# Optimization experiments

Measured on AMD Instinct MI355X. Metric: run time of the kernel, lower is better.

## Reference

```python
import jax, jax.numpy as jnp
import numpy as np

WIN = 32  # hardcoded window size in the original module


def _find(parent, x):
    while parent[x] != x:
        parent[x] = parent[parent[x]]
        x = parent[x]
    return x


def _label_background(bg):
    # 4-connected component labeling of True pixels; False pixels get label 0
    w = bg.shape[0]
    n = w * w
    parent = np.arange(n, dtype=np.int64)
    flat = bg.ravel()
    idx = np.arange(n).reshape(w, w)
    e1 = np.concatenate([idx[:, :-1].ravel(), idx[:-1, :].ravel()])
    e2 = np.concatenate([idx[:, 1:].ravel(), idx[1:, :].ravel()])
    for a, b in zip(e1, e2):
        if flat[a] and flat[b]:
            ra, rb = _find(parent, a), _find(parent, b)
            if ra != rb:
                parent[ra] = rb
    labels = np.zeros(n, dtype=np.int64)
    root2lab = {}
    nxt = 1
    for i in range(n):
        if flat[i]:
            r = _find(parent, i)
            if r not in root2lab:
                root2lab[r] = nxt
                nxt += 1
            labels[i] = root2lab[r]
    return labels


def _malis(seg, e1, e2, costs, pos):
    # Kruskal-style maximin MALIS edge weighting (descending affinity order).
    # Pairs involving segment label 0 (foreground / non-background) are excluded.
    n = seg.shape[0]
    parent = np.arange(n, dtype=np.int64)
    cnts = [({int(seg[i]): 1} if seg[i] != 0 else {}) for i in range(n)]
    w = np.zeros(costs.shape[0], dtype=np.int64)
    order = np.argsort(-costs, kind='stable')
    for e in order:
        a, b = _find(parent, e1[e]), _find(parent, e2[e])
        if a == b:
            continue
        ca, cb = cnts[a], cnts[b]
        if len(ca) > len(cb):  # small-to-large merge
            a, b, ca, cb = b, a, cb, ca
        common = 0
        for l, c in ca.items():
            if l in cb:
                common += c * cb[l]
        if pos:
            w[e] = common
        else:
            sa = sum(ca.values())
            sb = sum(cb.values())
            w[e] = sa * sb - common
        for l, c in ca.items():
            cb[l] = cb.get(l, 0) + c
        parent[a] = b
        cnts[a] = {}
    return w


def _malis_weights_full(pred, target):
    pred = np.asarray(pred)
    target = np.asarray(target)
    B, C, H, W = pred.shape
    weights_n = np.zeros(pred.shape, dtype=np.float32)
    weights_p = np.zeros(pred.shape, dtype=np.float32)
    idx = np.arange(WIN * WIN).reshape(WIN, WIN)
    e1 = np.concatenate([idx[:, :-1].ravel(), idx[:-1, :].ravel()])
    e2 = np.concatenate([idx[:, 1:].ravel(), idx[1:, :].ravel()])
    for r in range(H // WIN):
        for c in range(W // WIN):
            p = pred[:, :, r * WIN:(r + 1) * WIN, c * WIN:(c + 1) * WIN]
            t = target[:, :, r * WIN:(r + 1) * WIN, c * WIN:(c + 1) * WIN]
            costs_h = (p[:, :, :, :-1] + p[:, :, :, 1:]).reshape(B, -1)
            costs_v = (p[:, :, :-1, :] + p[:, :, 1:, :]).reshape(B, -1)
            costs = np.concatenate([costs_h, costs_v], 1)
            gt_h = (t[:, :, :, :-1] + t[:, :, :, 1:]).reshape(B, -1)
            gt_v = (t[:, :, :-1, :] + t[:, :, 1:, :]).reshape(B, -1)
            gt = np.concatenate([gt_h, gt_v], 1)
            costs_n = costs.copy()
            costs_p = costs.copy()
            costs_n[gt > 20] = 20
            costs_p[gt < 10] = 0
            gt = np.minimum(gt, 20)
            for i in range(B):
                seg = _label_background(t[i, 0] == 0)
                wn = _malis(seg, e1, e2, costs_n[i].astype(np.float32), 0).astype(np.float64)
                wp = _malis(seg, e1, e2, costs_p[i].astype(np.float32), 1).astype(np.float64)
                if wn.sum() > 0:
                    wn = wn / wn.sum()
                if wp.sum() > 0:
                    wp = wp / wp.sum()
                wn[gt[i] >= 10] = 0
                wp[gt[i] < 20] = 0
                half = WIN * (WIN - 1)
                for wsrc, wdst in ((wn, weights_n), (wp, weights_p)):
                    wh = wsrc[:half].reshape(WIN, WIN - 1)
                    wv = wsrc[half:].reshape(WIN - 1, WIN)
                    nw = np.zeros((WIN, WIN), dtype=np.float64)
                    nw[:, :-1] += wh
                    nw[:, 1:] += wh
                    nw[:-1, :] += wv
                    nw[1:, :] += wv
                    wdst[i, 0, r * WIN:(r + 1) * WIN, c * WIN:(c + 1) * WIN] = nw
    return weights_n, weights_p


def setup_inputs() -> dict:
    key = jax.random.key(0)
    k1, k2 = jax.random.split(key)
    y_true = jax.random.randint(k1, (4, 1, 256, 256), 0, 2).astype(jnp.float32) * 20.0
    y_pred = jax.random.uniform(k2, (4, 1, 256, 256), dtype=jnp.float32) * 20.0
    return {"y_true": y_true, "y_pred": y_pred}


def reference(y_true, y_pred):
    malis_lr = 1.0
    malis_lr_pos = 1.0
    out_sd = (jax.ShapeDtypeStruct(y_pred.shape, jnp.float32),
              jax.ShapeDtypeStruct(y_pred.shape, jnp.float32))
    weights_n, weights_p = jax.pure_callback(
        _malis_weights_full, out_sd,
        jax.lax.stop_gradient(y_pred), jax.lax.stop_gradient(y_true))
    loss_n = y_pred ** 2
    loss_p = (20.0 - y_pred) ** 2
    return (malis_lr * loss_n * weights_n + malis_lr_pos * loss_p * weights_p).sum()
```

## Files before the change

### kernel.cpp

```cpp
#include <hip/hip_runtime.h>

#define NPIX   1024
#define NEH    992
#define NEDGE  1984
#define SORTN  2048
#define CHUNK  8
#define NMERGE 1023
#define NIL    0xFFFFu

#define MRG_STRIDE 20480
#define MRG_M      0
#define MRG_RA     256
#define MRG_RB     4608
#define MRG_SS     8960
#define MRG_ED     13312
#define MRG_NXT    15616

__device__ __forceinline__ void edge_ab(int e, int& a, int& b) {
    if (e < NEH) { int y = e / 31; int x = e - y * 31; a = y * 32 + x; b = a + 1; }
    else         { int ev = e - NEH; a = ev; b = ev + 32; }
}

__device__ __forceinline__ uint4 add4(uint4 x, uint4 y) {
    return make_uint4(x.x + y.x, x.y + y.y, x.z + y.z, x.w + y.w);
}
__device__ __forceinline__ uint4 sub4(uint4 x, uint4 y) {
    return make_uint4(x.x - y.x, x.y - y.y, x.z - y.z, x.w - y.w);
}

__device__ void ccl_body(char* smem, int* kprimeSh,
                         const float* __restrict__ t_glob,
                         unsigned short* __restrict__ pixLab_g,
                         int* __restrict__ Kg, int tileId) {
    const int tid = threadIdx.x;
    const int bat = tileId >> 6;
    const int tile = tileId & 63;
    const int tr = tile >> 3, tc = tile & 7;

    unsigned short* labS = (unsigned short*)smem;
    unsigned int*   cntS = (unsigned int*)(smem + 2048);
    unsigned char*  bgS  = (unsigned char*)(smem + 20480);

    for (int i = tid; i < NPIX; i += 256) {
        int y = i >> 5, x = i & 31;
        int gidx = bat * 65536 + (tr * 32 + y) * 256 + (tc * 32 + x);
        bgS[i] = (t_glob[gidx] == 0.0f) ? 1 : 0;
    }
    __syncthreads();

    if (tid < 64) {
        const int lane = tid;
        if (lane < 32) {
            #pragma unroll
            for (int x = 0; x < 32; x++) {
                int i = lane * 32 + x;
                labS[i] = bgS[i] ? (unsigned short)i : (unsigned short)NIL;
            }
        }
        while (true) {
            bool changed = false;
            if (lane < 32) {
                const int base = lane * 32;
                unsigned short v[32];
                #pragma unroll
                for (int x = 0; x < 32; x++) v[x] = labS[base + x];
                unsigned run = NIL;
                #pragma unroll
                for (int x = 0; x < 32; x++) {
                    unsigned val = v[x];
                    if (val == NIL) { run = NIL; }
                    else { unsigned nv = min(run, val); changed |= (nv != val); v[x] = (unsigned short)nv; run = nv; }
                }
                run = NIL;
                #pragma unroll
                for (int x = 31; x >= 0; x--) {
                    unsigned val = v[x];
                    if (val == NIL) { run = NIL; }
                    else { unsigned nv = min(run, val); changed |= (nv != val); v[x] = (unsigned short)nv; run = nv; }
                }
                #pragma unroll
                for (int x = 0; x < 32; x++) labS[base + x] = v[x];
            }
            if (lane < 32) {
                unsigned short c[32];
                #pragma unroll
                for (int k = 0; k < 32; k++) c[k] = labS[k * 32 + lane];
                unsigned run = NIL;
                #pragma unroll
                for (int k = 0; k < 32; k++) {
                    unsigned val = c[k];
                    if (val == NIL) { run = NIL; }
                    else { unsigned nv = min(run, val); changed |= (nv != val); c[k] = (unsigned short)nv; run = nv; }
                }
                run = NIL;
                #pragma unroll
                for (int k = 31; k >= 0; k--) {
                    unsigned val = c[k];
                    if (val == NIL) { run = NIL; }
                    else { unsigned nv = min(run, val); changed |= (nv != val); c[k] = (unsigned short)nv; run = nv; }
                }
                #pragma unroll
                for (int k = 0; k < 32; k++) labS[k * 32 + lane] = c[k];
            }
            if (!__any(changed)) break;
        }
    }
    __syncthreads();

    for (int i = tid; i < NPIX; i += 256) cntS[i] = 0;
    if (tid == 0) *kprimeSh = 0;
    __syncthreads();
    for (int i = tid; i < NPIX; i += 256)
        if (bgS[i]) atomicAdd(&cntS[labS[i]], 1u);
    __syncthreads();
    for (int i = tid; i < NPIX; i += 256) {
        if (bgS[i] && (int)labS[i] == i) {
            unsigned id = (cntS[i] >= 2) ? (unsigned)atomicAdd(kprimeSh, 1) : NIL;
            cntS[i] = id;
        }
    }
    __syncthreads();
    for (int i = tid; i < NPIX; i += 256)
        pixLab_g[tileId * NPIX + i] = bgS[i] ? (unsigned short)cntS[labS[i]] : (unsigned short)NIL;
    if (tid == 0) Kg[tileId] = *kprimeSh;
}

__device__ void sort_body(char* smem,
                          const float* __restrict__ t_glob,
                          const float* __restrict__ p_glob,
                          unsigned short* __restrict__ ord_g, int wg) {
    const int tid = threadIdx.x;
    const int sgn = wg & 1;
    const int tileId = wg >> 1;
    const int bat = tileId >> 6;
    const int tile = tileId & 63;
    const int tr = tile >> 3, tc = tile & 7;

    float*              pT   = (float*)smem;
    unsigned long long* keys = (unsigned long long*)(smem + 4096);
    unsigned char*      bgS  = (unsigned char*)(smem + 20480);

    for (int i = tid; i < NPIX; i += 256) {
        int y = i >> 5, x = i & 31;
        int gidx = bat * 65536 + (tr * 32 + y) * 256 + (tc * 32 + x);
        pT[i] = p_glob[gidx];
        bgS[i] = (t_glob[gidx] == 0.0f) ? 1 : 0;
    }
    __syncthreads();

    for (int k = tid; k < SORTN; k += 256) {
        unsigned long long key = 0ULL;
        if (k < NEDGE) {
            int a, b; edge_ab(k, a, b);
            float cost = pT[a] + pT[b];
            int nfg = (int)(!bgS[a]) + (int)(!bgS[b]);
            if (sgn == 0) { if (nfg == 2) cost = 20.0f; }
            else          { if (nfg == 0) cost = 0.0f;  }
            key = ((unsigned long long)__float_as_uint(cost) << 16)
                | (unsigned long long)(0xFFFFu - (unsigned)k);
        }
        keys[k] = key;
    }
    __syncthreads();
    for (int kk = 2; kk <= SORTN; kk <<= 1) {
        for (int jj = kk >> 1; jj > 0; jj >>= 1) {
            for (int i = tid; i < SORTN; i += 256) {
                int ixj = i ^ jj;
                if (ixj > i) {
                    unsigned long long A = keys[i], Bv = keys[ixj];
                    bool descBlk = ((i & kk) == 0);
                    if ((A < Bv) == descBlk) { keys[i] = Bv; keys[ixj] = A; }
                }
            }
            __syncthreads();
        }
    }
    for (int k = tid; k < NEDGE; k += 256)
        ord_g[(size_t)wg * SORTN + k] = (unsigned short)(0xFFFFu - (unsigned)(keys[k] & 0xFFFFULL));
}

__global__ __launch_bounds__(256, 2)
void k12_ccl_sort(const float* __restrict__ t_glob,
                  const float* __restrict__ p_glob,
                  unsigned short* __restrict__ pixLab_g,
                  int* __restrict__ Kg,
                  unsigned short* __restrict__ ord_g,
                  int nT) {
    __shared__ __align__(16) char smem[21504];
    __shared__ int kprimeSh;
    if ((int)blockIdx.x < nT)
        ccl_body(smem, &kprimeSh, t_glob, pixLab_g, Kg, blockIdx.x);
    else
        sort_body(smem, t_glob, p_glob, ord_g, blockIdx.x - nT);
}

__global__ __launch_bounds__(64)
void k3_kruskal(const float* __restrict__ t_glob,
                const unsigned short* __restrict__ ord_g,
                char* __restrict__ mrg_base) {
    const int lane = threadIdx.x;
    const int wg  = blockIdx.x;
    const int tileId = wg >> 1;
    const int bat = tileId >> 6;
    const int tile = tileId & 63;
    const int tr = tile >> 3, tc = tile & 7;

    __shared__ unsigned short parentS[NPIX];
    __shared__ unsigned long long nodeS[NPIX];
    __shared__ unsigned short nextS[NPIX];
    __shared__ unsigned int   claimS[NPIX];

    char* mg = mrg_base + (size_t)wg * MRG_STRIDE;
    unsigned int*   mrA = (unsigned int*)(mg + MRG_RA);
    unsigned int*   mrB = (unsigned int*)(mg + MRG_RB);
    unsigned int*   mSS = (unsigned int*)(mg + MRG_SS);
    unsigned short* mED = (unsigned short*)(mg + MRG_ED);
    unsigned short* mNX = (unsigned short*)(mg + MRG_NXT);
    const unsigned short* ord = ord_g + (size_t)wg * SORTN;

    for (int i = lane; i < NPIX; i += 64) {
        int y = i >> 5, x = i & 31;
        int gidx = bat * 65536 + (tr * 32 + y) * 256 + (tc * 32 + x);
        unsigned bg = (t_glob[gidx] == 0.0f) ? 1u : 0u;
        parentS[i] = (unsigned short)i;
        nodeS[i] = ((unsigned long long)i << 48) | ((unsigned long long)i << 32)
                 | (1ULL << 16) | (unsigned long long)bg;
        nextS[i] = (unsigned short)NIL;
    }
    __syncthreads();

    int m = 0;
    for (int kb = 0; kb < NEDGE; kb += 64) {
        int e = ord[kb + lane];
        int a, b; edge_ab(e, a, b);
        unsigned ra = (unsigned)a, rb = (unsigned)b;
        bool pending = true;
        bool committed = false;
        unsigned recA = 0, recB = 0, recSS = 0;

        while (__any(pending)) {
            if (pending) {
                while (true) {
                    unsigned pa = parentS[ra];
                    unsigned pb = parentS[rb];
                    if (pa == ra && pb == rb) break;
                    if (pa != ra) { unsigned ga = parentS[pa]; parentS[ra] = (unsigned short)ga; ra = ga; }
                    if (pb != rb) { unsigned gb = parentS[pb]; parentS[rb] = (unsigned short)gb; rb = gb; }
                }
                if (ra == rb) pending = false;
            }
            if (pending) {
                claimS[ra] = 0xFFFFFFFFu;
                claimS[rb] = 0xFFFFFFFFu;
            }
            if (pending) {
                atomicMin(&claimS[ra], (unsigned)lane);
                atomicMin(&claimS[rb], (unsigned)lane);
            }
            bool win = pending && (claimS[ra] == (unsigned)lane) && (claimS[rb] == (unsigned)lane);
            if (win) {
                unsigned long long nA = nodeS[ra], nB = nodeS[rb];
                unsigned cons = ra, surv = rb;
                unsigned szAu = (unsigned)(nA >> 16) & 0xFFFFu;
                unsigned szBu = (unsigned)(nB >> 16) & 0xFFFFu;
                if (szAu > szBu) {
                    unsigned t = cons; cons = surv; surv = t;
                    unsigned long long tn = nA; nA = nB; nB = tn;
                }
                unsigned headA = (unsigned)(nA >> 48);
                unsigned tailA = (unsigned)(nA >> 32) & 0xFFFFu;
                unsigned szA   = (unsigned)(nA >> 16) & 0xFFFFu;
                unsigned slA   = (unsigned)nA & 0xFFFFu;
                unsigned headB = (unsigned)(nB >> 48);
                unsigned tailB = (unsigned)(nB >> 32) & 0xFFFFu;
                unsigned szB   = (unsigned)(nB >> 16) & 0xFFFFu;
                unsigned slB   = (unsigned)nB & 0xFFFFu;
                unsigned long long merged =
                      ((unsigned long long)headA << 48)
                    | ((unsigned long long)tailB << 32)
                    | ((unsigned long long)(szA + szB) << 16)
                    | (unsigned long long)(slA + slB);
                parentS[cons] = (unsigned short)surv;
                nodeS[surv]   = merged;
                nextS[tailA]  = (unsigned short)headB;
                recA = (headA << 16) | headB;
                recB = (szA << 16) | szB;
                recSS = slA * slB;
                committed = true;
                pending = false;
            }
        }
        unsigned long long cm = __ballot(committed);
        if (committed) {
            int idx = m + (int)__popcll(cm & ((1ULL << lane) - 1ULL));
            mrA[idx] = recA;
            mrB[idx] = recB;
            mSS[idx] = recSS;
            mED[idx] = (unsigned short)e;
        }
        m += (int)__popcll(cm);
    }
    if (lane == 0) *(int*)(mg + MRG_M) = m;
    for (int i = lane; i < NPIX; i += 64) mNX[i] = nextS[i];
}

__global__ __launch_bounds__(256, 2)
void k4_weights(const float* __restrict__ t_glob,
                const float* __restrict__ p_glob,
                const unsigned short* __restrict__ pixLab_g,
                const int* __restrict__ Kg,
                const char* __restrict__ mrg_base,
                float* __restrict__ out) {
    const int tid = threadIdx.x;
    const int wg  = blockIdx.x;
    const int sgn = wg & 1;
    const int tileId = wg >> 1;
    const int bat = tileId >> 6;
    const int tile = tileId & 63;
    const int tr = tile >> 3, tc = tile & 7;

    __shared__ float          pT[NPIX];
    __shared__ unsigned char  bgS[NPIX];
    __shared__ unsigned short pixLab[NPIX];
    __shared__ unsigned short posS[NPIX];
    __shared__ unsigned int   mRecA[NMERGE];
    __shared__ unsigned int   mRecB[NMERGE];
    __shared__ unsigned int   mSaSb[NMERGE];
    __shared__ unsigned int   commonW[NMERGE];
    __shared__ unsigned short mEd[NMERGE];
    __shared__ __align__(16) unsigned long long big[2564];
    __shared__ unsigned wsumSh;
    __shared__ float lossSh;

    const char* mg = mrg_base + (size_t)wg * MRG_STRIDE;
    const int M = *(const int*)(mg + MRG_M);
    const int K = Kg[tileId];
    const unsigned int*   mrA = (const unsigned int*)(mg + MRG_RA);
    const unsigned int*   mrB = (const unsigned int*)(mg + MRG_RB);
    const unsigned int*   mSS = (const unsigned int*)(mg + MRG_SS);
    const unsigned short* mED = (const unsigned short*)(mg + MRG_ED);
    const unsigned short* mNX = (const unsigned short*)(mg + MRG_NXT);

    for (int i = tid; i < NPIX; i += 256) {
        int y = i >> 5, x = i & 31;
        int gidx = bat * 65536 + (tr * 32 + y) * 256 + (tc * 32 + x);
        pT[i] = p_glob[gidx];
        bgS[i] = (t_glob[gidx] == 0.0f) ? 1 : 0;
        pixLab[i] = pixLab_g[tileId * NPIX + i];
    }
    for (int j = tid; j < M; j += 256) {
        mRecA[j] = mrA[j];
        mRecB[j] = mrB[j];
        mSaSb[j] = mSS[j];
        mEd[j]   = mED[j];
        commonW[j] = 0;
    }

    unsigned short* n0 = (unsigned short*)big;
    unsigned short* n1 = n0 + 1024;
    unsigned short* d0 = n0 + 2048;
    unsigned short* d1 = n0 + 3072;
    for (int i = tid; i < NPIX; i += 256) { n0[i] = mNX[i]; d0[i] = 1; }
    __syncthreads();
    for (int s = 0; s < 10; s++) {
        unsigned short* sn = (s & 1) ? n1 : n0;
        unsigned short* sd = (s & 1) ? d1 : d0;
        unsigned short* dn = (s & 1) ? n0 : n1;
        unsigned short* dd = (s & 1) ? d0 : d1;
        for (int i = tid; i < NPIX; i += 256) {
            unsigned nx = sn[i];
            unsigned dv = sd[i];
            if (nx != NIL) { dv += sd[nx]; nx = sn[nx]; }
            dn[i] = (unsigned short)nx;
            dd[i] = (unsigned short)dv;
        }
        __syncthreads();
    }
    for (int i = tid; i < NPIX; i += 256)
        posS[i] = (unsigned short)(NPIX - (int)d0[i]);
    __syncthreads();

    unsigned*       P32 = (unsigned*)big;
    uint4*          P4  = (uint4*)big;
    unsigned*       scr = P32 + 4100;
    uint4*          S4  = (uint4*)scr;
    unsigned short* P16 = (unsigned short*)big;
    for (int base = 0; base < K; base += CHUNK) {
        for (int idx = tid; idx < 4100; idx += 256) P32[idx] = 0;
        __syncthreads();
        for (int i = tid; i < NPIX; i += 256) {
            unsigned l = pixLab[i];
            if (l != NIL && l >= (unsigned)base && l < (unsigned)(base + CHUNK))
                P16[(posS[i] + 1) * 8 + (l - base)] = 1;
        }
        __syncthreads();
        {
            int r0 = tid * 4 + 1;
            uint4 acc = P4[r0];
            for (int rr = r0 + 1; rr <= r0 + 3; rr++) { acc = add4(acc, P4[rr]); P4[rr] = acc; }
            S4[tid] = acc;
            __syncthreads();
            if (tid < 64) {
                uint4 s0 = S4[tid * 4], s1 = S4[tid * 4 + 1], s2 = S4[tid * 4 + 2], s3 = S4[tid * 4 + 3];
                uint4 t1 = add4(s0, s1), t2 = add4(t1, s2), t3 = add4(t2, s3);
                uint4 run = t3;
                #pragma unroll
                for (int d = 1; d < 64; d <<= 1) {
                    uint4 o;
                    o.x = __shfl_up(run.x, d, 64);
                    o.y = __shfl_up(run.y, d, 64);
                    o.z = __shfl_up(run.z, d, 64);
                    o.w = __shfl_up(run.w, d, 64);
                    if (tid >= d) run = add4(run, o);
                }
                uint4 off = sub4(run, t3);
                S4[tid * 4]     = add4(s0, off);
                S4[tid * 4 + 1] = add4(t1, off);
                S4[tid * 4 + 2] = add4(t2, off);
                S4[tid * 4 + 3] = add4(t3, off);
            }
            __syncthreads();
            if (tid > 0) {
                uint4 off = S4[tid - 1];
                for (int rr = r0; rr <= r0 + 3; rr++) P4[rr] = add4(P4[rr], off);
            }
        }
        __syncthreads();
        for (int j = tid; j < M; j += 256) {
            unsigned recA = mRecA[j], recB = mRecB[j];
            unsigned aS = posS[recA >> 16];
            unsigned bS = posS[recA & 0xFFFFu];
            uint4 da = sub4(P4[aS + (recB >> 16)], P4[aS]);
            uint4 db = sub4(P4[bS + (recB & 0xFFFFu)], P4[bS]);
            unsigned acc;
            acc  = (da.x & 0xFFFFu) * (db.x & 0xFFFFu) + (da.x >> 16) * (db.x >> 16);
            acc += (da.y & 0xFFFFu) * (db.y & 0xFFFFu) + (da.y >> 16) * (db.y >> 16);
            acc += (da.z & 0xFFFFu) * (db.z & 0xFFFFu) + (da.z >> 16) * (db.z >> 16);
            acc += (da.w & 0xFFFFu) * (db.w & 0xFFFFu) + (da.w >> 16) * (db.w >> 16);
            commonW[j] += acc;
        }
        __syncthreads();
    }

    if (tid == 0) { wsumSh = 0; lossSh = 0.0f; }
    __syncthreads();
    unsigned wloc = 0;
    for (int j = tid; j < M; j += 256)
        wloc += (sgn == 0) ? (mSaSb[j] - commonW[j]) : commonW[j];
    if (wloc) atomicAdd(&wsumSh, wloc);
    __syncthreads();
    const unsigned wsum = wsumSh;
    if (wsum > 0) {
        const double inv = 1.0 / (double)wsum;
        float lloc = 0.0f;
        for (int j = tid; j < M; j += 256) {
            unsigned w = (sgn == 0) ? (mSaSb[j] - commonW[j]) : commonW[j];
            if (!w) continue;
            int e = mEd[j];
            int a, b; edge_ab(e, a, b);
            int nfg = (int)(!bgS[a]) + (int)(!bgS[b]);
            bool keep = (sgn == 0) ? (nfg == 0) : (nfg >= 1);
            if (!keep) continue;
            float wn = (float)((double)w * inv);
            float fa, fb;
            if (sgn == 0) { fa = pT[a] * pT[a];            fb = pT[b] * pT[b]; }
            else { float da = 20.0f - pT[a], db = 20.0f - pT[b]; fa = da * da; fb = db * db; }
            lloc += wn * (fa + fb);
        }
        if (lloc != 0.0f) atomicAdd(&lossSh, lloc);
        __syncthreads();
        if (tid == 0 && lossSh != 0.0f) atomicAdd(out, lossSh);
    }
}

__global__ __launch_bounds__(256, 2)
void malis_mono(const float* __restrict__ t_glob,
                const float* __restrict__ p_glob,
                float* __restrict__ out) {
    const int tid  = threadIdx.x;
    const int wg   = blockIdx.x;
    const int sgn  = wg & 1;
    const int tileId = wg >> 1;
    const int bat  = tileId >> 6;
    const int tile = tileId & 63;
    const int tr = tile >> 3, tc = tile & 7;

    __shared__ float          pT[NPIX];
    __shared__ unsigned char  bgS[NPIX];
    __shared__ unsigned short pixLab[NPIX];
    __shared__ unsigned short parentS[NPIX];
    __shared__ unsigned short nextS[NPIX];
    __shared__ unsigned long long nodeS[NPIX];
    __shared__ unsigned int   claimS[NPIX];
    __shared__ unsigned short posS[NPIX];
    __shared__ unsigned short orderS[NEDGE];
    __shared__ unsigned int   mRecA[NMERGE];
    __shared__ unsigned int   mRecB[NMERGE];
    __shared__ unsigned short mEd[NMERGE];
    __shared__ unsigned int   mSaSb[NMERGE];
    __shared__ unsigned int   commonW[NMERGE];
    __shared__ __align__(16) unsigned long long big[2564];
    __shared__ int   kprimeSh, mCountSh;
    __shared__ unsigned wsumSh;
    __shared__ float lossSh;

    for (int i = tid; i < NPIX; i += 256) {
        int y = i >> 5, x = i & 31;
        int gidx = bat * 65536 + (tr * 32 + y) * 256 + (tc * 32 + x);
        pT[i] = p_glob[gidx];
        bgS[i] = (t_glob[gidx] == 0.0f) ? 1 : 0;
    }
    __syncthreads();

    unsigned short* labS = (unsigned short*)big;
    unsigned int*   cntS = (unsigned int*)(((char*)big) + 2048);
    if (tid < 64) {
        const int lane = tid;
        if (lane < 32) {
            #pragma unroll
            for (int x = 0; x < 32; x++) {
                int i = lane * 32 + x;
                labS[i] = bgS[i] ? (unsigned short)i : (unsigned short)NIL;
            }
        }
        while (true) {
            bool changed = false;
            if (lane < 32) {
                const int base = lane * 32;
                unsigned short v[32];
                #pragma unroll
                for (int x = 0; x < 32; x++) v[x] = labS[base + x];
                unsigned run = NIL;
                #pragma unroll
                for (int x = 0; x < 32; x++) {
                    unsigned val = v[x];
                    if (val == NIL) { run = NIL; }
                    else { unsigned nv = min(run, val); changed |= (nv != val); v[x] = (unsigned short)nv; run = nv; }
                }
                run = NIL;
                #pragma unroll
                for (int x = 31; x >= 0; x--) {
                    unsigned val = v[x];
                    if (val == NIL) { run = NIL; }
                    else { unsigned nv = min(run, val); changed |= (nv != val); v[x] = (unsigned short)nv; run = nv; }
                }
                #pragma unroll
                for (int x = 0; x < 32; x++) labS[base + x] = v[x];
            }
            if (lane < 32) {
                unsigned short c[32];
                #pragma unroll
                for (int k = 0; k < 32; k++) c[k] = labS[k * 32 + lane];
                unsigned run = NIL;
                #pragma unroll
                for (int k = 0; k < 32; k++) {
                    unsigned val = c[k];
                    if (val == NIL) { run = NIL; }
                    else { unsigned nv = min(run, val); changed |= (nv != val); c[k] = (unsigned short)nv; run = nv; }
                }
                run = NIL;
                #pragma unroll
                for (int k = 31; k >= 0; k--) {
                    unsigned val = c[k];
                    if (val == NIL) { run = NIL; }
                    else { unsigned nv = min(run, val); changed |= (nv != val); c[k] = (unsigned short)nv; run = nv; }
                }
                #pragma unroll
                for (int k = 0; k < 32; k++) labS[k * 32 + lane] = c[k];
            }
            if (!__any(changed)) break;
        }
    }
    __syncthreads();

    for (int i = tid; i < NPIX; i += 256) cntS[i] = 0;
    if (tid == 0) kprimeSh = 0;
    __syncthreads();
    for (int i = tid; i < NPIX; i += 256)
        if (bgS[i]) atomicAdd(&cntS[labS[i]], 1u);
    __syncthreads();
    for (int i = tid; i < NPIX; i += 256) {
        if (bgS[i] && (int)labS[i] == i) {
            unsigned id = (cntS[i] >= 2) ? (unsigned)atomicAdd(&kprimeSh, 1) : NIL;
            cntS[i] = id;
        }
    }
    __syncthreads();
    for (int i = tid; i < NPIX; i += 256)
        pixLab[i] = bgS[i] ? (unsigned short)cntS[labS[i]] : (unsigned short)NIL;
    __syncthreads();
    const int K = kprimeSh;

    unsigned long long* keys = big;
    for (int k = tid; k < SORTN; k += 256) {
        unsigned long long key = 0ULL;
        if (k < NEDGE) {
            int a, b; edge_ab(k, a, b);
            float cost = pT[a] + pT[b];
            int nfg = (int)(!bgS[a]) + (int)(!bgS[b]);
            if (sgn == 0) { if (nfg == 2) cost = 20.0f; }
            else          { if (nfg == 0) cost = 0.0f;  }
            key = ((unsigned long long)__float_as_uint(cost) << 16)
                | (unsigned long long)(0xFFFFu - (unsigned)k);
        }
        keys[k] = key;
    }
    __syncthreads();
    for (int kk = 2; kk <= SORTN; kk <<= 1) {
        for (int jj = kk >> 1; jj > 0; jj >>= 1) {
            for (int i = tid; i < SORTN; i += 256) {
                int ixj = i ^ jj;
                if (ixj > i) {
                    unsigned long long A = keys[i], Bv = keys[ixj];
                    bool descBlk = ((i & kk) == 0);
                    if ((A < Bv) == descBlk) { keys[i] = Bv; keys[ixj] = A; }
                }
            }
            __syncthreads();
        }
    }
    for (int k = tid; k < NEDGE; k += 256)
        orderS[k] = (unsigned short)(0xFFFFu - (unsigned)(keys[k] & 0xFFFFULL));
    for (int i = tid; i < NPIX; i += 256) {
        parentS[i] = (unsigned short)i;
        nodeS[i] = ((unsigned long long)i << 48) | ((unsigned long long)i << 32)
                 | (1ULL << 16) | (unsigned long long)bgS[i];
        nextS[i] = (unsigned short)NIL;
    }
    __syncthreads();

    if (tid < 64) {
        const int lane = tid;
        int m = 0;
        for (int kb = 0; kb < NEDGE; kb += 64) {
            int e = orderS[kb + lane];
            int a, b; edge_ab(e, a, b);
            unsigned ra = (unsigned)a, rb = (unsigned)b;
            bool pending = true;
            bool committed = false;
            unsigned recA = 0, recB = 0, recSS = 0;
            while (__any(pending)) {
                if (pending) {
                    while (true) {
                        unsigned pa = parentS[ra];
                        unsigned pb = parentS[rb];
                        if (pa == ra && pb == rb) break;
                        if (pa != ra) { unsigned ga = parentS[pa]; parentS[ra] = (unsigned short)ga; ra = ga; }
                        if (pb != rb) { unsigned gb = parentS[pb]; parentS[rb] = (unsigned short)gb; rb = gb; }
                    }
                    if (ra == rb) pending = false;
                }
                if (pending) {
                    claimS[ra] = 0xFFFFFFFFu;
                    claimS[rb] = 0xFFFFFFFFu;
                }
                if (pending) {
                    atomicMin(&claimS[ra], (unsigned)lane);
                    atomicMin(&claimS[rb], (unsigned)lane);
                }
                bool win = pending && (claimS[ra] == (unsigned)lane) && (claimS[rb] == (unsigned)lane);
                if (win) {
                    unsigned long long nA = nodeS[ra], nB = nodeS[rb];
                    unsigned cons = ra, surv = rb;
                    unsigned szAu = (unsigned)(nA >> 16) & 0xFFFFu;
                    unsigned szBu = (unsigned)(nB >> 16) & 0xFFFFu;
                    if (szAu > szBu) {
                        unsigned t = cons; cons = surv; surv = t;
                        unsigned long long tn = nA; nA = nB; nB = tn;
                    }
                    unsigned headA = (unsigned)(nA >> 48);
                    unsigned tailA = (unsigned)(nA >> 32) & 0xFFFFu;
                    unsigned szA   = (unsigned)(nA >> 16) & 0xFFFFu;
                    unsigned slA   = (unsigned)nA & 0xFFFFu;
                    unsigned headB = (unsigned)(nB >> 48);
                    unsigned tailB = (unsigned)(nB >> 32) & 0xFFFFu;
                    unsigned szB   = (unsigned)(nB >> 16) & 0xFFFFu;
                    unsigned slB   = (unsigned)nB & 0xFFFFu;
                    unsigned long long merged =
                          ((unsigned long long)headA << 48)
                        | ((unsigned long long)tailB << 32)
                        | ((unsigned long long)(szA + szB) << 16)
                        | (unsigned long long)(slA + slB);
                    parentS[cons] = (unsigned short)surv;
                    nodeS[surv]   = merged;
                    nextS[tailA]  = (unsigned short)headB;
                    recA = (headA << 16) | headB;
                    recB = (szA << 16) | szB;
                    recSS = slA * slB;
                    committed = true;
                    pending = false;
                }
            }
            unsigned long long cm = __ballot(committed);
            if (committed) {
                int idx = m + (int)__popcll(cm & ((1ULL << lane) - 1ULL));
                mRecA[idx] = recA;
                mRecB[idx] = recB;
                mSaSb[idx] = recSS;
                mEd[idx]   = (unsigned short)e;
            }
            m += (int)__popcll(cm);
        }
        if (lane == 0) mCountSh = m;
    }
    __syncthreads();
    const int M = mCountSh;
    for (int j = tid; j < M; j += 256) commonW[j] = 0;

    unsigned short* n0 = (unsigned short*)big;
    unsigned short* n1 = n0 + 1024;
    unsigned short* d0 = n0 + 2048;
    unsigned short* d1 = n0 + 3072;
    for (int i = tid; i < NPIX; i += 256) { n0[i] = nextS[i]; d0[i] = 1; }
    __syncthreads();
    for (int s = 0; s < 10; s++) {
        unsigned short* sn = (s & 1) ? n1 : n0;
        unsigned short* sd = (s & 1) ? d1 : d0;
        unsigned short* dn = (s & 1) ? n0 : n1;
        unsigned short* dd = (s & 1) ? d0 : d1;
        for (int i = tid; i < NPIX; i += 256) {
            unsigned nx = sn[i];
            unsigned dv = sd[i];
            if (nx != NIL) { dv += sd[nx]; nx = sn[nx]; }
            dn[i] = (unsigned short)nx;
            dd[i] = (unsigned short)dv;
        }
        __syncthreads();
    }
    for (int i = tid; i < NPIX; i += 256)
        posS[i] = (unsigned short)(NPIX - (int)d0[i]);
    __syncthreads();

    unsigned*       P32 = (unsigned*)big;
    uint4*          P4  = (uint4*)big;
    unsigned*       scr = P32 + 4100;
    uint4*          S4  = (uint4*)scr;
    unsigned short* P16 = (unsigned short*)big;
    for (int base = 0; base < K; base += CHUNK) {
        for (int idx = tid; idx < 4100; idx += 256) P32[idx] = 0;
        __syncthreads();
        for (int i = tid; i < NPIX; i += 256) {
            unsigned l = pixLab[i];
            if (l != NIL && l >= (unsigned)base && l < (unsigned)(base + CHUNK))
                P16[(posS[i] + 1) * 8 + (l - base)] = 1;
        }
        __syncthreads();
        {
            int r0 = tid * 4 + 1;
            uint4 acc = P4[r0];
            for (int rr = r0 + 1; rr <= r0 + 3; rr++) { acc = add4(acc, P4[rr]); P4[rr] = acc; }
            S4[tid] = acc;
            __syncthreads();
            if (tid < 64) {
                uint4 s0 = S4[tid * 4], s1 = S4[tid * 4 + 1], s2 = S4[tid * 4 + 2], s3 = S4[tid * 4 + 3];
                uint4 t1 = add4(s0, s1), t2 = add4(t1, s2), t3 = add4(t2, s3);
                uint4 run = t3;
                #pragma unroll
                for (int d = 1; d < 64; d <<= 1) {
                    uint4 o;
                    o.x = __shfl_up(run.x, d, 64);
                    o.y = __shfl_up(run.y, d, 64);
                    o.z = __shfl_up(run.z, d, 64);
                    o.w = __shfl_up(run.w, d, 64);
                    if (tid >= d) run = add4(run, o);
                }
                uint4 off = sub4(run, t3);
                S4[tid * 4]     = add4(s0, off);
                S4[tid * 4 + 1] = add4(t1, off);
                S4[tid * 4 + 2] = add4(t2, off);
                S4[tid * 4 + 3] = add4(t3, off);
            }
            __syncthreads();
            if (tid > 0) {
                uint4 off = S4[tid - 1];
                for (int rr = r0; rr <= r0 + 3; rr++) P4[rr] = add4(P4[rr], off);
            }
        }
        __syncthreads();
        for (int j = tid; j < M; j += 256) {
            unsigned recA = mRecA[j], recB = mRecB[j];
            unsigned aS = posS[recA >> 16];
            unsigned bS = posS[recA & 0xFFFFu];
            uint4 da = sub4(P4[aS + (recB >> 16)], P4[aS]);
            uint4 db = sub4(P4[bS + (recB & 0xFFFFu)], P4[bS]);
            unsigned acc;
            acc  = (da.x & 0xFFFFu) * (db.x & 0xFFFFu) + (da.x >> 16) * (db.x >> 16);
            acc += (da.y & 0xFFFFu) * (db.y & 0xFFFFu) + (da.y >> 16) * (db.y >> 16);
            acc += (da.z & 0xFFFFu) * (db.z & 0xFFFFu) + (da.z >> 16) * (db.z >> 16);
            acc += (da.w & 0xFFFFu) * (db.w & 0xFFFFu) + (da.w >> 16) * (db.w >> 16);
            commonW[j] += acc;
        }
        __syncthreads();
    }

    if (tid == 0) { wsumSh = 0; lossSh = 0.0f; }
    __syncthreads();
    unsigned wloc = 0;
    for (int j = tid; j < M; j += 256)
        wloc += (sgn == 0) ? (mSaSb[j] - commonW[j]) : commonW[j];
    if (wloc) atomicAdd(&wsumSh, wloc);
    __syncthreads();
    const unsigned wsum = wsumSh;
    if (wsum > 0) {
        const double inv = 1.0 / (double)wsum;
        float lloc = 0.0f;
        for (int j = tid; j < M; j += 256) {
            unsigned w = (sgn == 0) ? (mSaSb[j] - commonW[j]) : commonW[j];
            if (!w) continue;
            int e = mEd[j];
            int a, b; edge_ab(e, a, b);
            int nfg = (int)(!bgS[a]) + (int)(!bgS[b]);
            bool keep = (sgn == 0) ? (nfg == 0) : (nfg >= 1);
            if (!keep) continue;
            float wn = (float)((double)w * inv);
            float fa, fb;
            if (sgn == 0) { fa = pT[a] * pT[a];            fb = pT[b] * pT[b]; }
            else { float da = 20.0f - pT[a], db = 20.0f - pT[b]; fa = da * da; fb = db * db; }
            lloc += wn * (fa + fb);
        }
        if (lloc != 0.0f) atomicAdd(&lossSh, lloc);
        __syncthreads();
        if (tid == 0 && lossSh != 0.0f) atomicAdd(out, lossSh);
    }
}

extern "C" void kernel_launch(void* const* d_in, const int* in_sizes, int n_in,
                              void* d_out, int out_size, void* d_ws, size_t ws_size,
                              hipStream_t stream) {
    const float* y_true = (const float*)d_in[0];
    const float* y_pred = (const float*)d_in[1];
    float* out = (float*)d_out;
    const int B  = in_sizes[0] / (256 * 256);
    const int nT = B * 64;
    const int nW = nT * 2;

    const size_t offK   = (size_t)nT * 2048;
    const size_t offOrd = offK + (((size_t)nT * 4 + 255) & ~(size_t)255);
    const size_t offMrg = offOrd + (size_t)nW * 4096;
    const size_t need   = offMrg + (size_t)nW * MRG_STRIDE;

    hipMemsetAsync(d_out, 0, (size_t)out_size * sizeof(float), stream);

    if (ws_size >= need) {
        char* ws = (char*)d_ws;
        unsigned short* pixLab_g = (unsigned short*)ws;
        int*            Kg       = (int*)(ws + offK);
        unsigned short* ord_g    = (unsigned short*)(ws + offOrd);
        char*           mrg      = ws + offMrg;
        hipLaunchKernelGGL(k12_ccl_sort, dim3(nT + nW), dim3(256), 0, stream,
                           y_true, y_pred, pixLab_g, Kg, ord_g, nT);
        hipLaunchKernelGGL(k3_kruskal,   dim3(nW), dim3(64),  0, stream, y_true, ord_g, mrg);
        hipLaunchKernelGGL(k4_weights,   dim3(nW), dim3(256), 0, stream, y_true, y_pred,
                           pixLab_g, Kg, mrg, out);
    } else {
        hipLaunchKernelGGL(malis_mono, dim3(nW), dim3(256), 0, stream, y_true, y_pred, out);
    }
}
```

Baseline: 311.3 us.

## Resolve low-contention union-find conflicts serially with register-resident merge log

The wave-parallel Kruskal merge loop now exits its claim/retry rounds once fewer than six lanes win per round. The remaining pending edges are processed serially in edge order through readlane broadcasts, and a per-lane log of recent merges (root remaps and node data) lets later edges see earlier merges without re-walking shared memory. The aim is to stop long tails of nearly serial conflict rounds, each of which pays LDS atomics and a path-compression pass. The cost is a serial loop with several ballots per edge. Correctness relies on the log holding up to 64 entries and on chained root remapping, which only follows one level.

After: 297.6 us. -4.4%, faster.

```diff
diff --git a/kernel.cpp b/kernel.cpp
--- a/kernel.cpp
+++ b/kernel.cpp
@@ -26,6 +26,15 @@
 }
 __device__ __forceinline__ uint4 sub4(uint4 x, uint4 y) {
     return make_uint4(x.x - y.x, x.y - y.y, x.z - y.z, x.w - y.w);
+}
+
+__device__ __forceinline__ unsigned rdl32(unsigned v, int lane) {
+    return (unsigned)__builtin_amdgcn_readlane((int)v, lane);
+}
+__device__ __forceinline__ unsigned long long rdl64(unsigned long long v, int lane) {
+    unsigned lo = (unsigned)__builtin_amdgcn_readlane((int)(unsigned)v, lane);
+    unsigned hi = (unsigned)__builtin_amdgcn_readlane((int)(unsigned)(v >> 32), lane);
+    return ((unsigned long long)hi << 32) | lo;
 }
 
 __device__ void ccl_body(char* smem, int* kprimeSh,
@@ -234,21 +243,19 @@
         int e = ord[kb + lane];
         int a, b; edge_ab(e, a, b);
         unsigned ra = (unsigned)a, rb = (unsigned)b;
-        bool pending = true;
+        while (true) {
+            unsigned pa = parentS[ra];
+            unsigned pb = parentS[rb];
+            if (pa == ra && pb == rb) break;
+            if (pa != ra) { unsigned ga = parentS[pa]; parentS[ra] = (unsigned short)ga; ra = ga; }
+            if (pb != rb) { unsigned gb = parentS[pb]; parentS[rb] = (unsigned short)gb; rb = gb; }
+        }
+        bool pending = (ra != rb);
         bool committed = false;
         unsigned recA = 0, recB = 0, recSS = 0;
 
-        while (__any(pending)) {
-            if (pending) {
-                while (true) {
-                    unsigned pa = parentS[ra];
-                    unsigned pb = parentS[rb];
-                    if (pa == ra && pb == rb) break;
-                    if (pa != ra) { unsigned ga = parentS[pa]; parentS[ra] = (unsigned short)ga; ra = ga; }
-                    if (pb != rb) { unsigned gb = parentS[pb]; parentS[rb] = (unsigned short)gb; rb = gb; }
-                }
-                if (ra == rb) pending = false;
-            }
+        int winners = 64;
+        while (__any(pending) && winners >= 6) {
             if (pending) {
                 claimS[ra] = 0xFFFFFFFFu;
                 claimS[rb] = 0xFFFFFFFFu;
@@ -289,16 +296,91 @@
                 committed = true;
                 pending = false;
             }
-        }
-        unsigned long long cm = __ballot(committed);
+            winners = (int)__popcll(__ballot(win));
+            if (pending) {
+                while (true) {
+                    unsigned pa = parentS[ra];
+                    unsigned pb = parentS[rb];
+                    if (pa == ra && pb == rb) break;
+                    if (pa != ra) { unsigned ga = parentS[pa]; parentS[ra] = (unsigned short)ga; ra = ga; }
+                    if (pb != rb) { unsigned gb = parentS[pb]; parentS[rb] = (unsigned short)gb; rb = gb; }
+                }
+                if (ra == rb) pending = false;
+            }
+        }
+
+        unsigned long long cmB = __ballot(committed);
         if (committed) {
-            int idx = m + (int)__popcll(cm & ((1ULL << lane) - 1ULL));
+            int idx = m + (int)__popcll(cmB & ((1ULL << lane) - 1ULL));
             mrA[idx] = recA;
             mrB[idx] = recB;
             mSS[idx] = recSS;
             mED[idx] = (unsigned short)e;
         }
-        m += (int)__popcll(cm);
+        int bulkCount = (int)__popcll(cmB);
+
+        int logCount = 0;
+        if (__any(pending)) {
+            unsigned long long na = 0, nb = 0;
+            if (pending) { na = nodeS[ra]; nb = nodeS[rb]; }
+            unsigned specAB = (ra << 16) | rb;
+            unsigned long long candm = __ballot(pending);
+            unsigned logRa  = 0xFFFFFFFFu;
+            unsigned logRbO = 0xFFFFFFFFu;
+            unsigned curRoot = 0xFFFFFFFFu;
+            unsigned long long logNode = 0;
+            while (candm != 0ULL) {
+                int j = __ffsll((long long)candm) - 1;
+                candm &= candm - 1ULL;
+                unsigned sAB = rdl32(specAB, j);
+                unsigned cra = sAB >> 16;
+                unsigned crb = sAB & 0xFFFFu;
+                unsigned long long hitA = __ballot(logRa == cra);
+                unsigned long long hitB = __ballot(logRa == crb);
+                if (hitA) cra = rdl32(curRoot, __ffsll((long long)hitA) - 1);
+                if (hitB) crb = rdl32(curRoot, __ffsll((long long)hitB) - 1);
+                if (cra == crb) continue;
+                unsigned ce = rdl32((unsigned)e, j);
+                unsigned long long hbA = __ballot(logRbO == cra);
+                unsigned long long hbB = __ballot(logRbO == crb);
+                unsigned long long cna = hbA ? rdl64(logNode, 63 - __clzll((long long)hbA)) : rdl64(na, j);
+                unsigned long long cnb = hbB ? rdl64(logNode, 63 - __clzll((long long)hbB)) : rdl64(nb, j);
+                unsigned cons = cra, surv = crb;
+                unsigned szAq = (unsigned)(cna >> 16) & 0xFFFFu;
+                unsigned szBq = (unsigned)(cnb >> 16) & 0xFFFFu;
+                if (szAq > szBq) {
+                    unsigned t = cons; cons = surv; surv = t;
+                    unsigned long long tn = cna; cna = cnb; cnb = tn;
+                }
+                unsigned headA = (unsigned)(cna >> 48);
+                unsigned tailA = (unsigned)(cna >> 32) & 0xFFFFu;
+                unsigned szA   = (unsigned)(cna >> 16) & 0xFFFFu;
+                unsigned slA   = (unsigned)cna & 0xFFFFu;
+                unsigned headB = (unsigned)(cnb >> 48);
+                unsigned tailB = (unsigned)(cnb >> 32) & 0xFFFFu;
+                unsigned szB   = (unsigned)(cnb >> 16) & 0xFFFFu;
+                unsigned slB   = (unsigned)cnb & 0xFFFFu;
+                unsigned long long merged =
+                      ((unsigned long long)headA << 48)
+                    | ((unsigned long long)tailB << 32)
+                    | ((unsigned long long)(szA + szB) << 16)
+                    | (unsigned long long)(slA + slB);
+                if (curRoot == cons) curRoot = surv;
+                if (lane == logCount) {
+                    logRa = cons; logRbO = surv; curRoot = surv; logNode = merged;
+                    parentS[cons] = (unsigned short)surv;
+                    nodeS[surv]   = merged;
+                    nextS[tailA]  = (unsigned short)headB;
+                    int idx = m + bulkCount + logCount;
+                    mrA[idx] = (headA << 16) | headB;
+                    mrB[idx] = (szA << 16) | szB;
+                    mSS[idx] = slA * slB;
+                    mED[idx] = (unsigned short)ce;
+                }
+                logCount++;
+            }
+        }
+        m += bulkCount + logCount;
     }
     if (lane == 0) *(int*)(mg + MRG_M) = m;
     for (int i = lane; i < NPIX; i += 64) mNX[i] = nextS[i];
```
